# Performance work log

Hardware: AMD Instinct MI355X
Metric: run time of the kernel (lower is better)

The kernel has to match this reference:

```python
import jax, jax.numpy as jnp
import numpy as np

EPS_INTERP = 1e-8
EPS_BN = 1e-5


def _bn_relu(x, gamma, beta):
    # x: [B, C, N]; training-mode BatchNorm1d over (B, N) with biased variance
    mean = jnp.mean(x, axis=(0, 2), keepdims=True)
    var = jnp.mean((x - mean) ** 2, axis=(0, 2), keepdims=True)
    xn = (x - mean) / jnp.sqrt(var + EPS_BN)
    return jax.nn.relu(xn * gamma[None, :, None] + beta[None, :, None])


def setup_inputs() -> dict:
    key = jax.random.key(0)
    ks = jax.random.split(key, 8)
    B, N, S, D = 16, 4096, 1024, 128
    return {
        "xyz1": jax.random.normal(ks[0], (B, 3, N), jnp.float32),
        "xyz2": jax.random.normal(ks[1], (B, 3, S), jnp.float32),
        "points1": jax.random.normal(ks[2], (B, D, N), jnp.float32),
        "points2": jax.random.normal(ks[3], (B, D, S), jnp.float32),
        "w0": jax.random.normal(ks[4], (256, 512), jnp.float32) * 0.04,
        "b0": jax.random.normal(ks[5], (256,), jnp.float32) * 0.01,
        "gamma0": jnp.ones((256,), jnp.float32),
        "beta0": jnp.zeros((256,), jnp.float32),
        "w1": jax.random.normal(ks[6], (128, 256), jnp.float32) * 0.06,
        "b1": jax.random.normal(ks[7], (128,), jnp.float32) * 0.01,
        "gamma1": jnp.ones((128,), jnp.float32),
        "beta1": jnp.zeros((128,), jnp.float32),
    }


def reference(xyz1, xyz2, points1, points2, w0, b0, gamma0, beta0, w1, b1, gamma1, beta1):
    # to [B, N, C] layouts
    x1 = jnp.transpose(xyz1, (0, 2, 1))   # [B, N, 3]
    x2 = jnp.transpose(xyz2, (0, 2, 1))   # [B, S, 3]
    p2 = jnp.transpose(points2, (0, 2, 1))  # [B, S, D]
    B, N, _ = x1.shape

    # squared pairwise distances [B, N, S]
    dists = (jnp.sum(x1 ** 2, -1)[:, :, None]
             + jnp.sum(x2 ** 2, -1)[:, None, :]
             - 2.0 * jnp.einsum('bnc,bsc->bns', x1, x2))

    # 3 nearest neighbors (ascending distance)
    neg_d, idx = jax.lax.top_k(-dists, 3)   # idx: [B, N, 3]
    d3 = -neg_d
    recip = 1.0 / (d3 + EPS_INTERP)
    weight = recip / jnp.sum(recip, axis=2, keepdims=True)  # [B, N, 3]

    # gather neighbor features: [B, N, 3, D]
    gathered = jax.vmap(lambda p, i: p[i])(p2, idx)
    # NOTE: this repo flattens the 3 weighted neighbors (no sum) -> [B, N, 3*D]
    interp = (gathered * weight[..., None]).reshape(B, N, -1)

    new_pts = jnp.concatenate([jnp.transpose(points1, (0, 2, 1)), interp], axis=-1)  # [B, N, 512]
    x = jnp.transpose(new_pts, (0, 2, 1))  # [B, 512, N]

    x = _bn_relu(jnp.einsum('oc,bcn->bon', w0, x) + b0[None, :, None], gamma0, beta0)
    x = _bn_relu(jnp.einsum('oc,bcn->bon', w1, x) + b1[None, :, None], gamma1, beta1)
    return x
```

## Files before the change

### kernel.cpp

```cpp
#include <hip/hip_runtime.h>
#include <stdint.h>

typedef unsigned short ushort_t;
typedef __attribute__((ext_vector_type(8))) __bf16 bf16x8;
typedef __attribute__((ext_vector_type(4))) float f32x4;

__device__ __forceinline__ float b2f(ushort_t u) {
    unsigned v = ((unsigned)u) << 16;
    float f;
    __builtin_memcpy(&f, &v, 4);
    return f;
}

__device__ __forceinline__ ushort_t f2b(float f) {
    __bf16 h = (__bf16)f;
    return __builtin_bit_cast(ushort_t, h);
}

__device__ __forceinline__ void gl_lds16(const void* g, void* l) {
    __builtin_amdgcn_global_load_lds((const __attribute__((address_space(1))) void*)g,
                                     (__attribute__((address_space(3))) void*)l, 16, 0, 0);
}

__global__ __launch_bounds__(256) void k_pre(const float* __restrict__ w0, ushort_t* __restrict__ w0b,
                                             const float* __restrict__ w1, ushort_t* __restrict__ w1b,
                                             const float* __restrict__ xyz2, float4* __restrict__ sdat,
                                             const float* __restrict__ points2, ushort_t* __restrict__ p2t,
                                             float* __restrict__ zb) {
    int bid = blockIdx.x;
    int t = threadIdx.x;
    if (bid < 512) {
        int i = bid * 256 + t;
        w0b[i] = f2b(w0[i]);
    } else if (bid < 640) {
        int i = (bid - 512) * 256 + t;
        w1b[i] = f2b(w1[i]);
    } else if (bid < 704) {
        int bb = bid - 640;
        int b = bb & 15, by = bb >> 4;
        int s = by * 256 + t;
        const float* x2 = xyz2 + (size_t)b * 3 * 1024;
        float x = x2[s], y = x2[1024 + s], z = x2[2048 + s];
        float4 v;
        v.x = x; v.y = y; v.z = z;
        v.w = __fadd_rn(__fadd_rn(__fmul_rn(x, x), __fmul_rn(y, y)), __fmul_rn(z, z));
        sdat[(size_t)b * 1024 + s] = v;
    } else if (bid < 960) {
        int bb = bid - 704;
        int b = bb & 15, sy = bb >> 4;
        int s = sy * 64 + (t & 63);
        int g = t >> 6;
        const float* src = points2 + (size_t)b * 128 * 1024 + s;
        ushort_t* dst = p2t + ((size_t)b * 1024 + s) * 128;
#pragma unroll
        for (int i = 0; i < 4; ++i) {
            int cp = i * 4 + g;
            ushort_t tmp[8];
#pragma unroll
            for (int k = 0; k < 8; ++k) tmp[k] = f2b(src[(size_t)(cp * 8 + k) * 1024]);
            *(uint4*)(dst + cp * 8) = *(const uint4*)tmp;
        }
    } else {
        zb[t] = 0.f; zb[256 + t] = 0.f;
        if (t < 128) { zb[512 + t] = 0.f; zb[640 + t] = 0.f; }
    }
}

__global__ __launch_bounds__(256) void k_interp(const float* __restrict__ xyz1,
                                                const float4* __restrict__ sdat,
                                                const float* __restrict__ points1,
                                                const ushort_t* __restrict__ p2t,
                                                ushort_t* __restrict__ X) {
    int b = blockIdx.x;
    int n0 = blockIdx.y * 32;
    int t = threadIdx.x;
    int tq = t & 31;
    int slice = t >> 5;
    int wave = t >> 6, lane = t & 63;

    __shared__ __align__(16) char sbuf[16384];
    float4* sP = (float4*)sbuf;
    int*   sidx = (int*)sbuf;
    float* sw   = (float*)(sbuf + 384);
    __shared__ float sD[768];
    __shared__ int   sI[768];

    {
        const float4* src = sdat + (size_t)b * 1024;
#pragma unroll
        for (int c = 0; c < 4; ++c) {
            int p = wave * 256 + c * 64 + lane;
            gl_lds16(src + p, sbuf + p * 16);
        }
    }

    int n = n0 + tq;
    float x = xyz1[((size_t)b * 3 + 0) * 4096 + n];
    float y = xyz1[((size_t)b * 3 + 1) * 4096 + n];
    float z = xyz1[((size_t)b * 3 + 2) * 4096 + n];
    float s1 = __fadd_rn(__fadd_rn(__fmul_rn(x, x), __fmul_rn(y, y)), __fmul_rn(z, z));

    __syncthreads();

    const float* p1base = points1 + (size_t)b * 128 * 4096 + n0 + tq;
    float p1v[16];
#pragma unroll
    for (int i = 0; i < 2; ++i)
#pragma unroll
        for (int k = 0; k < 8; ++k)
            p1v[i * 8 + k] = p1base[(size_t)(((i * 8 + slice) * 8) + k) * 4096];

    float d0 = 1e30f, d1 = 1e30f, d2 = 1e30f;
    int i0 = 0, i1 = 0, i2 = 0;
    int sbeg = slice * 128;
    const float4* sdL = sP + sbeg;
#pragma unroll 8
    for (int s = 0; s < 128; ++s) {
        float4 v = sdL[s];
        float dot = fmaf(z, v.z, fmaf(y, v.y, __fmul_rn(x, v.x)));
        float d = __fadd_rn(fmaf(-2.0f, dot, s1), v.w);
        int si = sbeg + s;
        bool c0 = d < d0, c1 = d < d1, c2 = d < d2;
        i2 = c1 ? i1 : (c2 ? si : i2);
        i1 = c0 ? i0 : (c1 ? si : i1);
        i0 = c0 ? si : i0;
        d2 = fminf(fmaxf(d, d1), d2);
        d1 = fminf(fmaxf(d, d0), d1);
        d0 = fminf(d, d0);
    }
    sD[t * 3 + 0] = d0; sD[t * 3 + 1] = d1; sD[t * 3 + 2] = d2;
    sI[t * 3 + 0] = i0; sI[t * 3 + 1] = i1; sI[t * 3 + 2] = i2;

    {
        ushort_t* dstbase = X + (size_t)(b * 4096 + n0 + tq) * 512;
#pragma unroll
        for (int i = 0; i < 2; ++i) {
            int piece = i * 8 + slice;
            ushort_t tmp[8];
#pragma unroll
            for (int k = 0; k < 8; ++k) tmp[k] = f2b(p1v[i * 8 + k]);
            *(uint4*)(dstbase + piece * 8) = *(const uint4*)tmp;
        }
    }
    __syncthreads();

    if (t < 32) {
        int sel0 = -1, sel1 = -1;
        float seld[3]; int seli[3];
#pragma unroll
        for (int r = 0; r < 3; ++r) {
            float bd = 1e38f; int bi = 1 << 30;
            for (int k = 0; k < 24; ++k) {
                int s3 = (k * 0xAAAB) >> 17;
                int rank = k - s3 * 3;
                int base = (s3 * 32 + t) * 3 + rank;
                float cd = sD[base];
                int ci = sI[base];
                bool excl = (ci == sel0) | (ci == sel1);
                bool better = (!excl) & ((cd < bd) | ((cd == bd) & (ci < bi)));
                if (better) { bd = cd; bi = ci; }
            }
            seld[r] = bd; seli[r] = bi;
            if (r == 0) sel0 = bi; else if (r == 1) sel1 = bi;
        }
        float r0 = 1.0f / (seld[0] + 1e-8f);
        float r1 = 1.0f / (seld[1] + 1e-8f);
        float r2 = 1.0f / (seld[2] + 1e-8f);
        float rs = r0 + r1 + r2;
        sw[t * 3 + 0] = r0 / rs; sw[t * 3 + 1] = r1 / rs; sw[t * 3 + 2] = r2 / rs;
        sidx[t * 3 + 0] = seli[0]; sidx[t * 3 + 1] = seli[1]; sidx[t * 3 + 2] = seli[2];
    }
    __syncthreads();

#pragma unroll
    for (int i = 0; i < 6; ++i) {
        int idx = i * 256 + t;
        int q = idx / 48;
        int rem = idx - q * 48;
        int r = rem >> 4;
        int piece = rem & 15;
        int si = sidx[q * 3 + r] & 1023;
        float wt = sw[q * 3 + r];
        const ushort_t* src = p2t + ((size_t)b * 1024 + si) * 128 + piece * 8;
        uint4 raw = *(const uint4*)src;
        ushort_t* e = (ushort_t*)&raw;
        ushort_t outv[8];
#pragma unroll
        for (int k = 0; k < 8; ++k) outv[k] = f2b(wt * b2f(e[k]));
        ushort_t* dst = X + (size_t)(b * 4096 + n0 + q) * 512 + 128 + r * 128 + piece * 8;
        *(uint4*)dst = *(const uint4*)outv;
    }
}

__global__ __launch_bounds__(512, 4) void k_gemm(const ushort_t* __restrict__ A,
                                                 const ushort_t* __restrict__ Bt,
                                                 const float* __restrict__ bias,
                                                 ushort_t* __restrict__ Y,
                                                 float* __restrict__ gs,
                                                 float* __restrict__ gq,
                                                 int Mtot, int K) {
    __shared__ __align__(16) char smem[51200];
    ushort_t* As = (ushort_t*)smem;
    ushort_t* Bs = (ushort_t*)(smem + 32768);
    ushort_t* sY = (ushort_t*)smem;
    float* red_s = (float*)(smem + 49152);
    float* red_q = red_s + 256;

    int t = threadIdx.x;
    int j0 = blockIdx.x * 128;
    int wave = t >> 6, lane = t & 63;
    int wm = wave >> 1, wn = wave & 1;
    int l16 = lane & 15, quad = lane >> 4;
    int sw7 = l16 & 7;

    if (t < 256) { red_s[t] = 0.f; red_q[t] = 0.f; }

    f32x4 acc[4][4] = {};

    int nk = K >> 6;
    for (int kt = 0; kt < nk; ++kt) {
#pragma unroll
        for (int c = 0; c < 4; ++c) {
            int idx = c * 512 + t;
            int row = idx >> 3, kc = idx & 7;
            gl_lds16(A + (size_t)row * K + kt * 64 + ((kc ^ (row & 7)) * 8), As + idx * 8);
        }
#pragma unroll
        for (int c = 0; c < 2; ++c) {
            int idx = c * 512 + t;
            int row = idx >> 3, kc = idx & 7;
            gl_lds16(Bt + (size_t)(j0 + row) * K + kt * 64 + ((kc ^ (row & 7)) * 8), Bs + idx * 8);
        }
        __syncthreads();

#pragma unroll
        for (int kk = 0; kk < 2; ++kk) {
            bf16x8 af[4], bfr[4];
#pragma unroll
            for (int mi = 0; mi < 4; ++mi)
                af[mi] = *(const bf16x8*)(As + (wm * 64 + mi * 16 + l16) * 64 + (((kk * 4 + quad) ^ sw7) * 8));
#pragma unroll
            for (int ni = 0; ni < 4; ++ni)
                bfr[ni] = *(const bf16x8*)(Bs + (wn * 64 + ni * 16 + l16) * 64 + (((kk * 4 + quad) ^ sw7) * 8));
#pragma unroll
            for (int mi = 0; mi < 4; ++mi)
#pragma unroll
                for (int ni = 0; ni < 4; ++ni)
                    acc[mi][ni] = __builtin_amdgcn_mfma_f32_16x16x32_bf16(af[mi], bfr[ni], acc[mi][ni], 0, 0, 0);
        }
        __syncthreads();
    }

#pragma unroll
    for (int h = 0; h < 2; ++h) {
        if ((wm >> 1) == h) {
#pragma unroll
            for (int mi = 0; mi < 4; ++mi) {
                int obase = wm * 64 + mi * 16 + quad * 4;
                int ocol = obase - h * 128;
                float bv[4];
#pragma unroll
                for (int r = 0; r < 4; ++r) bv[r] = bias[obase + r];
                float sr[4] = {0.f, 0.f, 0.f, 0.f}, qr[4] = {0.f, 0.f, 0.f, 0.f};
#pragma unroll
                for (int ni = 0; ni < 4; ++ni) {
                    int j_local = wn * 64 + ni * 16 + l16;
                    ushort4 pk;
                    float v0 = acc[mi][ni][0] + bv[0];
                    float v1 = acc[mi][ni][1] + bv[1];
                    float v2 = acc[mi][ni][2] + bv[2];
                    float v3 = acc[mi][ni][3] + bv[3];
                    pk.x = f2b(v0); pk.y = f2b(v1); pk.z = f2b(v2); pk.w = f2b(v3);
                    sr[0] += v0; qr[0] += v0 * v0;
                    sr[1] += v1; qr[1] += v1 * v1;
                    sr[2] += v2; qr[2] += v2 * v2;
                    sr[3] += v3; qr[3] += v3 * v3;
                    *(ushort4*)(sY + j_local * 136 + ocol) = pk;
                }
#pragma unroll
                for (int r = 0; r < 4; ++r) {
                    float s = sr[r], q = qr[r];
                    s += __shfl_xor(s, 1); s += __shfl_xor(s, 2);
                    s += __shfl_xor(s, 4); s += __shfl_xor(s, 8);
                    q += __shfl_xor(q, 1); q += __shfl_xor(q, 2);
                    q += __shfl_xor(q, 4); q += __shfl_xor(q, 8);
                    if (l16 == 0) {
                        atomicAdd(&red_s[obase + r], s);
                        atomicAdd(&red_q[obase + r], q);
                    }
                }
            }
        }
        __syncthreads();
#pragma unroll
        for (int rep = 0; rep < 4; ++rep) {
            int idx = rep * 512 + t;
            int jl = idx >> 4;
            int o8 = idx & 15;
            uint4 vv = *(const uint4*)(sY + jl * 136 + o8 * 8);
            *(uint4*)(Y + (size_t)(j0 + jl) * Mtot + h * 128 + o8 * 8) = vv;
        }
        __syncthreads();
    }
    if (t < 256) {
        atomicAdd(&gs[t], red_s[t]);
        atomicAdd(&gq[t], red_q[t]);
    }
}

__global__ __launch_bounds__(256) void k_gemmf(const ushort_t* __restrict__ A,
                                               const ushort_t* __restrict__ Y0,
                                               const float* __restrict__ bias,
                                               const float* __restrict__ gamma0,
                                               const float* __restrict__ beta0,
                                               const float* __restrict__ gs0,
                                               const float* __restrict__ gq0,
                                               ushort_t* __restrict__ Y,
                                               float* __restrict__ gs1,
                                               float* __restrict__ gq1,
                                               int Mtot, int K) {
    __shared__ __align__(16) char smem[35840];
    ushort_t* As = (ushort_t*)smem;
    ushort_t* Bs = (ushort_t*)(smem + 16384);
    float* sa = (float*)(smem + 32768);
    float* sb = (float*)(smem + 33792);
    ushort_t* sY = (ushort_t*)smem;
    float* red_s = (float*)(smem + 34816);
    float* red_q = red_s + 128;

    int t = threadIdx.x;
    int m0 = blockIdx.x * 128;
    int j0 = blockIdx.y * 128;
    int wave = t >> 6, lane = t & 63;
    int wm = wave >> 1, wn = wave & 1;
    int l16 = lane & 15, quad = lane >> 4;
    int sw7 = l16 & 7;

    {
        float s = gs0[t], q = gq0[t];
        float mean = s * (1.0f / 65536.0f);
        float var = q * (1.0f / 65536.0f) - mean * mean;
        float sc = gamma0[t] / sqrtf(var + 1e-5f);
        sa[t] = sc;
        sb[t] = beta0[t] - mean * sc;
    }
    if (t < 128) { red_s[t] = 0.f; red_q[t] = 0.f; }
    __syncthreads();

    f32x4 acc[4][4] = {};

    int nk = K >> 6;
    for (int kt = 0; kt < nk; ++kt) {
#pragma unroll
        for (int c = 0; c < 4; ++c) {
            int idx = c * 256 + t;
            int row = idx >> 3, kc = idx & 7;
            gl_lds16(A + (size_t)(m0 + row) * K + kt * 64 + ((kc ^ (row & 7)) * 8), As + idx * 8);
        }
#pragma unroll
        for (int c = 0; c < 4; ++c) {
            int idx = c * 256 + t;
            int row = idx >> 3, kc = idx & 7;
            int cbase = kt * 64 + kc * 8;
            uint4 raw = *(const uint4*)(Y0 + (size_t)(j0 + row) * K + cbase);
            ushort_t* e = (ushort_t*)&raw;
            ushort_t outv[8];
#pragma unroll
            for (int k = 0; k < 8; ++k) {
                float v = fmaxf(sa[cbase + k] * b2f(e[k]) + sb[cbase + k], 0.f);
                outv[k] = f2b(v);
            }
            *(uint4*)(Bs + row * 64 + ((kc ^ (row & 7)) * 8)) = *(const uint4*)outv;
        }
        __syncthreads();

#pragma unroll
        for (int kk = 0; kk < 2; ++kk) {
            bf16x8 af[4], bfr[4];
#pragma unroll
            for (int mi = 0; mi < 4; ++mi)
                af[mi] = *(const bf16x8*)(As + (wm * 64 + mi * 16 + l16) * 64 + (((kk * 4 + quad) ^ sw7) * 8));
#pragma unroll
            for (int ni = 0; ni < 4; ++ni)
                bfr[ni] = *(const bf16x8*)(Bs + (wn * 64 + ni * 16 + l16) * 64 + (((kk * 4 + quad) ^ sw7) * 8));
#pragma unroll
            for (int mi = 0; mi < 4; ++mi)
#pragma unroll
                for (int ni = 0; ni < 4; ++ni)
                    acc[mi][ni] = __builtin_amdgcn_mfma_f32_16x16x32_bf16(af[mi], bfr[ni], acc[mi][ni], 0, 0, 0);
        }
        __syncthreads();
    }

#pragma unroll
    for (int mi = 0; mi < 4; ++mi) {
        int obase = wm * 64 + mi * 16 + quad * 4;
        float bv[4];
#pragma unroll
        for (int r = 0; r < 4; ++r) bv[r] = bias[m0 + obase + r];
        float sr[4] = {0.f, 0.f, 0.f, 0.f}, qr[4] = {0.f, 0.f, 0.f, 0.f};
#pragma unroll
        for (int ni = 0; ni < 4; ++ni) {
            int j_local = wn * 64 + ni * 16 + l16;
            ushort4 pk;
            float v0 = acc[mi][ni][0] + bv[0];
            float v1 = acc[mi][ni][1] + bv[1];
            float v2 = acc[mi][ni][2] + bv[2];
            float v3 = acc[mi][ni][3] + bv[3];
            pk.x = f2b(v0); pk.y = f2b(v1); pk.z = f2b(v2); pk.w = f2b(v3);
            sr[0] += v0; qr[0] += v0 * v0;
            sr[1] += v1; qr[1] += v1 * v1;
            sr[2] += v2; qr[2] += v2 * v2;
            sr[3] += v3; qr[3] += v3 * v3;
            *(ushort4*)(sY + j_local * 136 + obase) = pk;
        }
#pragma unroll
        for (int r = 0; r < 4; ++r) {
            float s = sr[r], q = qr[r];
            s += __shfl_xor(s, 1); s += __shfl_xor(s, 2);
            s += __shfl_xor(s, 4); s += __shfl_xor(s, 8);
            q += __shfl_xor(q, 1); q += __shfl_xor(q, 2);
            q += __shfl_xor(q, 4); q += __shfl_xor(q, 8);
            if (l16 == 0) {
                atomicAdd(&red_s[obase + r], s);
                atomicAdd(&red_q[obase + r], q);
            }
        }
    }
    __syncthreads();

#pragma unroll
    for (int rep = 0; rep < 8; ++rep) {
        int idx = rep * 256 + t;
        int jl = idx >> 4;
        int o8 = idx & 15;
        uint4 vv = *(const uint4*)(sY + jl * 136 + o8 * 8);
        *(uint4*)(Y + (size_t)(j0 + jl) * Mtot + m0 + o8 * 8) = vv;
    }
    if (t < 128) {
        atomicAdd(&gs1[m0 + t], red_s[t]);
        atomicAdd(&gq1[m0 + t], red_q[t]);
    }
}

__global__ __launch_bounds__(256) void k_out(const ushort_t* __restrict__ Y1,
                                             const float* __restrict__ gs1,
                                             const float* __restrict__ gq1,
                                             const float* __restrict__ gamma1,
                                             const float* __restrict__ beta1,
                                             float* __restrict__ out) {
    __shared__ float sa[128], sb[128];
    int t = threadIdx.x;
    if (t < 128) {
        float s = gs1[t], q = gq1[t];
        float mean = s * (1.0f / 65536.0f);
        float var = q * (1.0f / 65536.0f) - mean * mean;
        float sc = gamma1[t] / sqrtf(var + 1e-5f);
        sa[t] = sc;
        sb[t] = beta1[t] - mean * sc;
    }
    __syncthreads();
    int b = blockIdx.x;
    int nl = t & 127;
    int half = t >> 7;
    int n = blockIdx.y * 128 + nl;
    const uint4* src = (const uint4*)(Y1 + (size_t)(b * 4096 + n) * 128);
    float* dst = out + (size_t)b * 128 * 4096 + n;
    uint4 raw[8];
#pragma unroll
    for (int p = 0; p < 8; ++p) raw[p] = src[half * 8 + p];
    const ushort_t* e = (const ushort_t*)raw;
#pragma unroll
    for (int c = 0; c < 64; ++c) {
        int ch = half * 64 + c;
        float v = b2f(e[c]);
        v = fmaxf(sa[ch] * v + sb[ch], 0.f);
        dst[(size_t)ch * 4096] = v;
    }
}

extern "C" void kernel_launch(void* const* d_in, const int* in_sizes, int n_in,
                              void* d_out, int out_size, void* d_ws, size_t ws_size,
                              hipStream_t stream) {
    const float* xyz1    = (const float*)d_in[0];
    const float* xyz2    = (const float*)d_in[1];
    const float* points1 = (const float*)d_in[2];
    const float* points2 = (const float*)d_in[3];
    const float* w0      = (const float*)d_in[4];
    const float* b0      = (const float*)d_in[5];
    const float* gamma0  = (const float*)d_in[6];
    const float* beta0   = (const float*)d_in[7];
    const float* w1      = (const float*)d_in[8];
    const float* b1      = (const float*)d_in[9];
    const float* gamma1  = (const float*)d_in[10];
    const float* beta1   = (const float*)d_in[11];
    float* out = (float*)d_out;

    char* ws = (char*)d_ws;
    const size_t OFF_X    = 0;
    const size_t OFF_Y0   = 67108864;
    const size_t OFF_Y1   = 100663296;
    const size_t OFF_P2T  = 117440512;
    const size_t OFF_W0B  = 121634816;
    const size_t OFF_W1B  = 121896960;
    const size_t OFF_AB   = 121962496;
    const size_t OFF_SDAT = 121965568;

    ushort_t* X    = (ushort_t*)(ws + OFF_X);
    ushort_t* Y0   = (ushort_t*)(ws + OFF_Y0);
    ushort_t* Y1   = (ushort_t*)(ws + OFF_Y1);
    ushort_t* p2t  = (ushort_t*)(ws + OFF_P2T);
    ushort_t* w0b  = (ushort_t*)(ws + OFF_W0B);
    ushort_t* w1b  = (ushort_t*)(ws + OFF_W1B);
    float* ab      = (float*)(ws + OFF_AB);
    float4* sdat   = (float4*)(ws + OFF_SDAT);
    float* gs0 = ab;        float* gq0 = ab + 256;
    float* gs1 = ab + 512;  float* gq1 = ab + 640;

    k_pre<<<961, 256, 0, stream>>>(w0, w0b, w1, w1b, xyz2, sdat, points2, p2t, ab);
    k_interp<<<dim3(16, 128), 256, 0, stream>>>(xyz1, sdat, points1, p2t, X);
    k_gemm<<<512, 512, 0, stream>>>(w0b, X, b0, Y0, gs0, gq0, 256, 512);
    k_gemmf<<<dim3(1, 512), 256, 0, stream>>>(w1b, Y0, b1, gamma0, beta0, gs0, gq0, Y1, gs1, gq1, 128, 256);
    k_out<<<dim3(16, 32), 256, 0, stream>>>(Y1, gs1, gq1, gamma1, beta1, out);
}
```

Measured before the change: 218.6 us.

## Halve GEMM column tiles and spread BN stat atomics over eight copies

Both GEMM kernels now use 64-column tiles instead of 128, which doubles the grid to 1024 blocks and shrinks LDS use so more blocks fit per CU. The first GEMM writes all 256 output rows in a single epilogue pass instead of two halves. BatchNorm sum and sum-of-squares atomics are spread across 8 copies indexed by block, and consumers add the copies together, to cut contention on the global atomics. The cost is less data reuse per tile (the weight tile is reloaded twice as often) and slightly more work to reduce the statistics.

```diff
diff --git a/kernel.cpp b/kernel.cpp
--- a/kernel.cpp
+++ b/kernel.cpp
@@ -61,8 +61,7 @@
             *(uint4*)(dst + cp * 8) = *(const uint4*)tmp;
         }
     } else {
-        zb[t] = 0.f; zb[256 + t] = 0.f;
-        if (t < 128) { zb[512 + t] = 0.f; zb[640 + t] = 0.f; }
+        for (int i = t; i < 6144; i += 256) zb[i] = 0.f;
     }
 }
 
@@ -192,22 +191,22 @@
     }
 }
 
-__global__ __launch_bounds__(512, 4) void k_gemm(const ushort_t* __restrict__ A,
+__global__ __launch_bounds__(512, 6) void k_gemm(const ushort_t* __restrict__ A,
                                                  const ushort_t* __restrict__ Bt,
                                                  const float* __restrict__ bias,
                                                  ushort_t* __restrict__ Y,
                                                  float* __restrict__ gs,
                                                  float* __restrict__ gq,
                                                  int Mtot, int K) {
-    __shared__ __align__(16) char smem[51200];
+    __shared__ __align__(16) char smem[43008];
     ushort_t* As = (ushort_t*)smem;
     ushort_t* Bs = (ushort_t*)(smem + 32768);
     ushort_t* sY = (ushort_t*)smem;
-    float* red_s = (float*)(smem + 49152);
+    float* red_s = (float*)(smem + 40960);
     float* red_q = red_s + 256;
 
     int t = threadIdx.x;
-    int j0 = blockIdx.x * 128;
+    int j0 = blockIdx.x * 64;
     int wave = t >> 6, lane = t & 63;
     int wm = wave >> 1, wn = wave & 1;
     int l16 = lane & 15, quad = lane >> 4;
@@ -215,7 +214,7 @@
 
     if (t < 256) { red_s[t] = 0.f; red_q[t] = 0.f; }
 
-    f32x4 acc[4][4] = {};
+    f32x4 acc[4][2] = {};
 
     int nk = K >> 6;
     for (int kt = 0; kt < nk; ++kt) {
@@ -225,9 +224,8 @@
             int row = idx >> 3, kc = idx & 7;
             gl_lds16(A + (size_t)row * K + kt * 64 + ((kc ^ (row & 7)) * 8), As + idx * 8);
         }
-#pragma unroll
-        for (int c = 0; c < 2; ++c) {
-            int idx = c * 512 + t;
+        {
+            int idx = t;
             int row = idx >> 3, kc = idx & 7;
             gl_lds16(Bt + (size_t)(j0 + row) * K + kt * 64 + ((kc ^ (row & 7)) * 8), Bs + idx * 8);
         }
@@ -235,109 +233,105 @@
 
 #pragma unroll
         for (int kk = 0; kk < 2; ++kk) {
-            bf16x8 af[4], bfr[4];
+            bf16x8 af[4], bfr[2];
 #pragma unroll
             for (int mi = 0; mi < 4; ++mi)
                 af[mi] = *(const bf16x8*)(As + (wm * 64 + mi * 16 + l16) * 64 + (((kk * 4 + quad) ^ sw7) * 8));
 #pragma unroll
-            for (int ni = 0; ni < 4; ++ni)
-                bfr[ni] = *(const bf16x8*)(Bs + (wn * 64 + ni * 16 + l16) * 64 + (((kk * 4 + quad) ^ sw7) * 8));
+            for (int ni = 0; ni < 2; ++ni)
+                bfr[ni] = *(const bf16x8*)(Bs + (wn * 32 + ni * 16 + l16) * 64 + (((kk * 4 + quad) ^ sw7) * 8));
 #pragma unroll
             for (int mi = 0; mi < 4; ++mi)
 #pragma unroll
-                for (int ni = 0; ni < 4; ++ni)
+                for (int ni = 0; ni < 2; ++ni)
                     acc[mi][ni] = __builtin_amdgcn_mfma_f32_16x16x32_bf16(af[mi], bfr[ni], acc[mi][ni], 0, 0, 0);
         }
         __syncthreads();
     }
 
 #pragma unroll
-    for (int h = 0; h < 2; ++h) {
-        if ((wm >> 1) == h) {
-#pragma unroll
-            for (int mi = 0; mi < 4; ++mi) {
-                int obase = wm * 64 + mi * 16 + quad * 4;
-                int ocol = obase - h * 128;
-                float bv[4];
-#pragma unroll
-                for (int r = 0; r < 4; ++r) bv[r] = bias[obase + r];
-                float sr[4] = {0.f, 0.f, 0.f, 0.f}, qr[4] = {0.f, 0.f, 0.f, 0.f};
-#pragma unroll
-                for (int ni = 0; ni < 4; ++ni) {
-                    int j_local = wn * 64 + ni * 16 + l16;
-                    ushort4 pk;
-                    float v0 = acc[mi][ni][0] + bv[0];
-                    float v1 = acc[mi][ni][1] + bv[1];
-                    float v2 = acc[mi][ni][2] + bv[2];
-                    float v3 = acc[mi][ni][3] + bv[3];
-                    pk.x = f2b(v0); pk.y = f2b(v1); pk.z = f2b(v2); pk.w = f2b(v3);
-                    sr[0] += v0; qr[0] += v0 * v0;
-                    sr[1] += v1; qr[1] += v1 * v1;
-                    sr[2] += v2; qr[2] += v2 * v2;
-                    sr[3] += v3; qr[3] += v3 * v3;
-                    *(ushort4*)(sY + j_local * 136 + ocol) = pk;
-                }
-#pragma unroll
-                for (int r = 0; r < 4; ++r) {
-                    float s = sr[r], q = qr[r];
-                    s += __shfl_xor(s, 1); s += __shfl_xor(s, 2);
-                    s += __shfl_xor(s, 4); s += __shfl_xor(s, 8);
-                    q += __shfl_xor(q, 1); q += __shfl_xor(q, 2);
-                    q += __shfl_xor(q, 4); q += __shfl_xor(q, 8);
-                    if (l16 == 0) {
-                        atomicAdd(&red_s[obase + r], s);
-                        atomicAdd(&red_q[obase + r], q);
-                    }
-                }
+    for (int mi = 0; mi < 4; ++mi) {
+        int obase = wm * 64 + mi * 16 + quad * 4;
+        float bv[4];
+#pragma unroll
+        for (int r = 0; r < 4; ++r) bv[r] = bias[obase + r];
+        float sr[4] = {0.f, 0.f, 0.f, 0.f}, qr[4] = {0.f, 0.f, 0.f, 0.f};
+#pragma unroll
+        for (int ni = 0; ni < 2; ++ni) {
+            int j_local = wn * 32 + ni * 16 + l16;
+            ushort4 pk;
+            float v0 = acc[mi][ni][0] + bv[0];
+            float v1 = acc[mi][ni][1] + bv[1];
+            float v2 = acc[mi][ni][2] + bv[2];
+            float v3 = acc[mi][ni][3] + bv[3];
+            pk.x = f2b(v0); pk.y = f2b(v1); pk.z = f2b(v2); pk.w = f2b(v3);
+            sr[0] += v0; qr[0] += v0 * v0;
+            sr[1] += v1; qr[1] += v1 * v1;
+            sr[2] += v2; qr[2] += v2 * v2;
+            sr[3] += v3; qr[3] += v3 * v3;
+            *(ushort4*)(sY + j_local * 264 + obase) = pk;
+        }
+#pragma unroll
+        for (int r = 0; r < 4; ++r) {
+            float s = sr[r], q = qr[r];
+            s += __shfl_xor(s, 1); s += __shfl_xor(s, 2);
+            s += __shfl_xor(s, 4); s += __shfl_xor(s, 8);
+            q += __shfl_xor(q, 1); q += __shfl_xor(q, 2);
+            q += __shfl_xor(q, 4); q += __shfl_xor(q, 8);
+            if (l16 == 0) {
+                atomicAdd(&red_s[obase + r], s);
+                atomicAdd(&red_q[obase + r], q);
             }
         }
-        __syncthreads();
-#pragma unroll
-        for (int rep = 0; rep < 4; ++rep) {
-            int idx = rep * 512 + t;
-            int jl = idx >> 4;
-            int o8 = idx & 15;
-            uint4 vv = *(const uint4*)(sY + jl * 136 + o8 * 8);
-            *(uint4*)(Y + (size_t)(j0 + jl) * Mtot + h * 128 + o8 * 8) = vv;
-        }
-        __syncthreads();
+    }
+    __syncthreads();
+
+#pragma unroll
+    for (int rep = 0; rep < 4; ++rep) {
+        int idx = rep * 512 + t;
+        int jl = idx >> 5;
+        int o8 = idx & 31;
+        uint4 vv = *(const uint4*)(sY + jl * 264 + o8 * 8);
+        *(uint4*)(Y + (size_t)(j0 + jl) * Mtot + o8 * 8) = vv;
     }
     if (t < 256) {
-        atomicAdd(&gs[t], red_s[t]);
-        atomicAdd(&gq[t], red_q[t]);
-    }
-}
-
-__global__ __launch_bounds__(256) void k_gemmf(const ushort_t* __restrict__ A,
-                                               const ushort_t* __restrict__ Y0,
-                                               const float* __restrict__ bias,
-                                               const float* __restrict__ gamma0,
-                                               const float* __restrict__ beta0,
-                                               const float* __restrict__ gs0,
-                                               const float* __restrict__ gq0,
-                                               ushort_t* __restrict__ Y,
-                                               float* __restrict__ gs1,
-                                               float* __restrict__ gq1,
-                                               int Mtot, int K) {
-    __shared__ __align__(16) char smem[35840];
+        int cp = blockIdx.x & 7;
+        atomicAdd(&gs[cp * 256 + t], red_s[t]);
+        atomicAdd(&gq[cp * 256 + t], red_q[t]);
+    }
+}
+
+__global__ __launch_bounds__(256, 4) void k_gemmf(const ushort_t* __restrict__ A,
+                                                  const ushort_t* __restrict__ Y0,
+                                                  const float* __restrict__ bias,
+                                                  const float* __restrict__ gamma0,
+                                                  const float* __restrict__ beta0,
+                                                  const float* __restrict__ gs0,
+                                                  const float* __restrict__ gq0,
+                                                  ushort_t* __restrict__ Y,
+                                                  float* __restrict__ gs1,
+                                                  float* __restrict__ gq1,
+                                                  int Mtot, int K) {
+    __shared__ __align__(16) char smem[27648];
     ushort_t* As = (ushort_t*)smem;
     ushort_t* Bs = (ushort_t*)(smem + 16384);
-    float* sa = (float*)(smem + 32768);
-    float* sb = (float*)(smem + 33792);
     ushort_t* sY = (ushort_t*)smem;
-    float* red_s = (float*)(smem + 34816);
+    float* sa = (float*)(smem + 24576);
+    float* sb = (float*)(smem + 25600);
+    float* red_s = (float*)(smem + 26624);
     float* red_q = red_s + 128;
 
     int t = threadIdx.x;
-    int m0 = blockIdx.x * 128;
-    int j0 = blockIdx.y * 128;
+    int j0 = blockIdx.x * 64;
     int wave = t >> 6, lane = t & 63;
     int wm = wave >> 1, wn = wave & 1;
     int l16 = lane & 15, quad = lane >> 4;
     int sw7 = l16 & 7;
 
     {
-        float s = gs0[t], q = gq0[t];
+        float s = 0.f, q = 0.f;
+#pragma unroll
+        for (int k = 0; k < 8; ++k) { s += gs0[k * 256 + t]; q += gq0[k * 256 + t]; }
         float mean = s * (1.0f / 65536.0f);
         float var = q * (1.0f / 65536.0f) - mean * mean;
         float sc = gamma0[t] / sqrtf(var + 1e-5f);
@@ -347,7 +341,7 @@
     if (t < 128) { red_s[t] = 0.f; red_q[t] = 0.f; }
     __syncthreads();
 
-    f32x4 acc[4][4] = {};
+    f32x4 acc[4][2] = {};
 
     int nk = K >> 6;
     for (int kt = 0; kt < nk; ++kt) {
@@ -355,10 +349,10 @@
         for (int c = 0; c < 4; ++c) {
             int idx = c * 256 + t;
             int row = idx >> 3, kc = idx & 7;
-            gl_lds16(A + (size_t)(m0 + row) * K + kt * 64 + ((kc ^ (row & 7)) * 8), As + idx * 8);
-        }
-#pragma unroll
-        for (int c = 0; c < 4; ++c) {
+            gl_lds16(A + (size_t)row * K + kt * 64 + ((kc ^ (row & 7)) * 8), As + idx * 8);
+        }
+#pragma unroll
+        for (int c = 0; c < 2; ++c) {
             int idx = c * 256 + t;
             int row = idx >> 3, kc = idx & 7;
             int cbase = kt * 64 + kc * 8;
@@ -376,17 +370,17 @@
 
 #pragma unroll
         for (int kk = 0; kk < 2; ++kk) {
-            bf16x8 af[4], bfr[4];
+            bf16x8 af[4], bfr[2];
 #pragma unroll
             for (int mi = 0; mi < 4; ++mi)
                 af[mi] = *(const bf16x8*)(As + (wm * 64 + mi * 16 + l16) * 64 + (((kk * 4 + quad) ^ sw7) * 8));
 #pragma unroll
-            for (int ni = 0; ni < 4; ++ni)
-                bfr[ni] = *(const bf16x8*)(Bs + (wn * 64 + ni * 16 + l16) * 64 + (((kk * 4 + quad) ^ sw7) * 8));
+            for (int ni = 0; ni < 2; ++ni)
+                bfr[ni] = *(const bf16x8*)(Bs + (wn * 32 + ni * 16 + l16) * 64 + (((kk * 4 + quad) ^ sw7) * 8));
 #pragma unroll
             for (int mi = 0; mi < 4; ++mi)
 #pragma unroll
-                for (int ni = 0; ni < 4; ++ni)
+                for (int ni = 0; ni < 2; ++ni)
                     acc[mi][ni] = __builtin_amdgcn_mfma_f32_16x16x32_bf16(af[mi], bfr[ni], acc[mi][ni], 0, 0, 0);
         }
         __syncthreads();
@@ -397,11 +391,11 @@
         int obase = wm * 64 + mi * 16 + quad * 4;
         float bv[4];
 #pragma unroll
-        for (int r = 0; r < 4; ++r) bv[r] = bias[m0 + obase + r];
+        for (int r = 0; r < 4; ++r) bv[r] = bias[obase + r];
         float sr[4] = {0.f, 0.f, 0.f, 0.f}, qr[4] = {0.f, 0.f, 0.f, 0.f};
 #pragma unroll
-        for (int ni = 0; ni < 4; ++ni) {
-            int j_local = wn * 64 + ni * 16 + l16;
+        for (int ni = 0; ni < 2; ++ni) {
+            int j_local = wn * 32 + ni * 16 + l16;
             ushort4 pk;
             float v0 = acc[mi][ni][0] + bv[0];
             float v1 = acc[mi][ni][1] + bv[1];
@@ -430,16 +424,17 @@
     __syncthreads();
 
 #pragma unroll
-    for (int rep = 0; rep < 8; ++rep) {
+    for (int rep = 0; rep < 4; ++rep) {
         int idx = rep * 256 + t;
         int jl = idx >> 4;
         int o8 = idx & 15;
         uint4 vv = *(const uint4*)(sY + jl * 136 + o8 * 8);
-        *(uint4*)(Y + (size_t)(j0 + jl) * Mtot + m0 + o8 * 8) = vv;
+        *(uint4*)(Y + (size_t)(j0 + jl) * Mtot + o8 * 8) = vv;
     }
     if (t < 128) {
-        atomicAdd(&gs1[m0 + t], red_s[t]);
-        atomicAdd(&gq1[m0 + t], red_q[t]);
+        int cp = blockIdx.x & 7;
+        atomicAdd(&gs1[cp * 128 + t], red_s[t]);
+        atomicAdd(&gq1[cp * 128 + t], red_q[t]);
     }
 }
 
@@ -452,7 +447,9 @@
     __shared__ float sa[128], sb[128];
     int t = threadIdx.x;
     if (t < 128) {
-        float s = gs1[t], q = gq1[t];
+        float s = 0.f, q = 0.f;
+#pragma unroll
+        for (int k = 0; k < 8; ++k) { s += gs1[k * 128 + t]; q += gq1[k * 128 + t]; }
         float mean = s * (1.0f / 65536.0f);
         float var = q * (1.0f / 65536.0f) - mean * mean;
         float sc = gamma1[t] / sqrtf(var + 1e-5f);
@@ -503,8 +500,8 @@
     const size_t OFF_P2T  = 117440512;
     const size_t OFF_W0B  = 121634816;
     const size_t OFF_W1B  = 121896960;
-    const size_t OFF_AB   = 121962496;
     const size_t OFF_SDAT = 121965568;
+    const size_t OFF_AB   = 122227712;
 
     ushort_t* X    = (ushort_t*)(ws + OFF_X);
     ushort_t* Y0   = (ushort_t*)(ws + OFF_Y0);
@@ -512,14 +509,14 @@
     ushort_t* p2t  = (ushort_t*)(ws + OFF_P2T);
     ushort_t* w0b  = (ushort_t*)(ws + OFF_W0B);
     ushort_t* w1b  = (ushort_t*)(ws + OFF_W1B);
+    float4* sdat   = (float4*)(ws + OFF_SDAT);
     float* ab      = (float*)(ws + OFF_AB);
-    float4* sdat   = (float4*)(ws + OFF_SDAT);
-    float* gs0 = ab;        float* gq0 = ab + 256;
-    float* gs1 = ab + 512;  float* gq1 = ab + 640;
+    float* gs0 = ab;               float* gq0 = ab + 2048;
+    float* gs1 = ab + 4096;        float* gq1 = ab + 5120;
 
     k_pre<<<961, 256, 0, stream>>>(w0, w0b, w1, w1b, xyz2, sdat, points2, p2t, ab);
     k_interp<<<dim3(16, 128), 256, 0, stream>>>(xyz1, sdat, points1, p2t, X);
-    k_gemm<<<512, 512, 0, stream>>>(w0b, X, b0, Y0, gs0, gq0, 256, 512);
-    k_gemmf<<<dim3(1, 512), 256, 0, stream>>>(w1b, Y0, b1, gamma0, beta0, gs0, gq0, Y1, gs1, gq1, 128, 256);
+    k_gemm<<<1024, 512, 0, stream>>>(w0b, X, b0, Y0, gs0, gq0, 256, 512);
+    k_gemmf<<<1024, 256, 0, stream>>>(w1b, Y0, b1, gamma0, beta0, gs0, gq0, Y1, gs1, gq1, 128, 256);
     k_out<<<dim3(16, 32), 256, 0, stream>>>(Y1, gs1, gq1, gamma1, beta1, out);
 }
```

Result: no change. 217.2 us (-0.7%).

## Spread BN stat atomics over 8 copies and drop LDS XOR swizzle

Applied to the files above, without the earlier changes.

The global BatchNorm sum and sum-of-squares accumulators are split into 8 copies indexed by block, and the consumers add the copies together. This is meant to reduce atomic contention on a single address per channel. Separately, the XOR swizzle on the LDS tiles in both GEMMs is removed in favour of plain row-major indexing, which simplifies address math but may bring back LDS bank conflicts on the 128-byte-stride fragment reads. The workspace layout is adjusted to hold the larger accumulator buffer, which k_pre now zeroes in a loop.

```diff
diff --git a/kernel.cpp b/kernel.cpp
--- a/kernel.cpp
+++ b/kernel.cpp
@@ -61,8 +61,7 @@
             *(uint4*)(dst + cp * 8) = *(const uint4*)tmp;
         }
     } else {
-        zb[t] = 0.f; zb[256 + t] = 0.f;
-        if (t < 128) { zb[512 + t] = 0.f; zb[640 + t] = 0.f; }
+        for (int i = t; i < 6144; i += 256) zb[i] = 0.f;
     }
 }
 
@@ -211,7 +210,6 @@
     int wave = t >> 6, lane = t & 63;
     int wm = wave >> 1, wn = wave & 1;
     int l16 = lane & 15, quad = lane >> 4;
-    int sw7 = l16 & 7;
 
     if (t < 256) { red_s[t] = 0.f; red_q[t] = 0.f; }
 
@@ -223,13 +221,13 @@
         for (int c = 0; c < 4; ++c) {
             int idx = c * 512 + t;
             int row = idx >> 3, kc = idx & 7;
-            gl_lds16(A + (size_t)row * K + kt * 64 + ((kc ^ (row & 7)) * 8), As + idx * 8);
+            gl_lds16(A + (size_t)row * K + kt * 64 + kc * 8, As + idx * 8);
         }
 #pragma unroll
         for (int c = 0; c < 2; ++c) {
             int idx = c * 512 + t;
             int row = idx >> 3, kc = idx & 7;
-            gl_lds16(Bt + (size_t)(j0 + row) * K + kt * 64 + ((kc ^ (row & 7)) * 8), Bs + idx * 8);
+            gl_lds16(Bt + (size_t)(j0 + row) * K + kt * 64 + kc * 8, Bs + idx * 8);
         }
         __syncthreads();
 
@@ -238,10 +236,10 @@
             bf16x8 af[4], bfr[4];
 #pragma unroll
             for (int mi = 0; mi < 4; ++mi)
-                af[mi] = *(const bf16x8*)(As + (wm * 64 + mi * 16 + l16) * 64 + (((kk * 4 + quad) ^ sw7) * 8));
+                af[mi] = *(const bf16x8*)(As + (wm * 64 + mi * 16 + l16) * 64 + kk * 32 + quad * 8);
 #pragma unroll
             for (int ni = 0; ni < 4; ++ni)
-                bfr[ni] = *(const bf16x8*)(Bs + (wn * 64 + ni * 16 + l16) * 64 + (((kk * 4 + quad) ^ sw7) * 8));
+                bfr[ni] = *(const bf16x8*)(Bs + (wn * 64 + ni * 16 + l16) * 64 + kk * 32 + quad * 8);
 #pragma unroll
             for (int mi = 0; mi < 4; ++mi)
 #pragma unroll
@@ -303,8 +301,9 @@
         __syncthreads();
     }
     if (t < 256) {
-        atomicAdd(&gs[t], red_s[t]);
-        atomicAdd(&gq[t], red_q[t]);
+        int cp = blockIdx.x & 7;
+        atomicAdd(&gs[cp * 256 + t], red_s[t]);
+        atomicAdd(&gq[cp * 256 + t], red_q[t]);
     }
 }
 
@@ -334,10 +333,11 @@
     int wave = t >> 6, lane = t & 63;
     int wm = wave >> 1, wn = wave & 1;
     int l16 = lane & 15, quad = lane >> 4;
-    int sw7 = l16 & 7;
 
     {
-        float s = gs0[t], q = gq0[t];
+        float s = 0.f, q = 0.f;
+#pragma unroll
+        for (int k = 0; k < 8; ++k) { s += gs0[k * 256 + t]; q += gq0[k * 256 + t]; }
         float mean = s * (1.0f / 65536.0f);
         float var = q * (1.0f / 65536.0f) - mean * mean;
         float sc = gamma0[t] / sqrtf(var + 1e-5f);
@@ -355,7 +355,7 @@
         for (int c = 0; c < 4; ++c) {
             int idx = c * 256 + t;
             int row = idx >> 3, kc = idx & 7;
-            gl_lds16(A + (size_t)(m0 + row) * K + kt * 64 + ((kc ^ (row & 7)) * 8), As + idx * 8);
+            gl_lds16(A + (size_t)(m0 + row) * K + kt * 64 + kc * 8, As + idx * 8);
         }
 #pragma unroll
         for (int c = 0; c < 4; ++c) {
@@ -370,7 +370,7 @@
                 float v = fmaxf(sa[cbase + k] * b2f(e[k]) + sb[cbase + k], 0.f);
                 outv[k] = f2b(v);
             }
-            *(uint4*)(Bs + row * 64 + ((kc ^ (row & 7)) * 8)) = *(const uint4*)outv;
+            *(uint4*)(Bs + idx * 8) = *(const uint4*)outv;
         }
         __syncthreads();
 
@@ -379,10 +379,10 @@
             bf16x8 af[4], bfr[4];
 #pragma unroll
             for (int mi = 0; mi < 4; ++mi)
-                af[mi] = *(const bf16x8*)(As + (wm * 64 + mi * 16 + l16) * 64 + (((kk * 4 + quad) ^ sw7) * 8));
+                af[mi] = *(const bf16x8*)(As + (wm * 64 + mi * 16 + l16) * 64 + kk * 32 + quad * 8);
 #pragma unroll
             for (int ni = 0; ni < 4; ++ni)
-                bfr[ni] = *(const bf16x8*)(Bs + (wn * 64 + ni * 16 + l16) * 64 + (((kk * 4 + quad) ^ sw7) * 8));
+                bfr[ni] = *(const bf16x8*)(Bs + (wn * 64 + ni * 16 + l16) * 64 + kk * 32 + quad * 8);
 #pragma unroll
             for (int mi = 0; mi < 4; ++mi)
 #pragma unroll
@@ -438,8 +438,9 @@
         *(uint4*)(Y + (size_t)(j0 + jl) * Mtot + m0 + o8 * 8) = vv;
     }
     if (t < 128) {
-        atomicAdd(&gs1[m0 + t], red_s[t]);
-        atomicAdd(&gq1[m0 + t], red_q[t]);
+        int cp = blockIdx.y & 7;
+        atomicAdd(&gs1[cp * 128 + m0 + t], red_s[t]);
+        atomicAdd(&gq1[cp * 128 + m0 + t], red_q[t]);
     }
 }
 
@@ -452,7 +453,9 @@
     __shared__ float sa[128], sb[128];
     int t = threadIdx.x;
     if (t < 128) {
-        float s = gs1[t], q = gq1[t];
+        float s = 0.f, q = 0.f;
+#pragma unroll
+        for (int k = 0; k < 8; ++k) { s += gs1[k * 128 + t]; q += gq1[k * 128 + t]; }
         float mean = s * (1.0f / 65536.0f);
         float var = q * (1.0f / 65536.0f) - mean * mean;
         float sc = gamma1[t] / sqrtf(var + 1e-5f);
@@ -503,8 +506,8 @@
     const size_t OFF_P2T  = 117440512;
     const size_t OFF_W0B  = 121634816;
     const size_t OFF_W1B  = 121896960;
-    const size_t OFF_AB   = 121962496;
     const size_t OFF_SDAT = 121965568;
+    const size_t OFF_AB   = 122227712;
 
     ushort_t* X    = (ushort_t*)(ws + OFF_X);
     ushort_t* Y0   = (ushort_t*)(ws + OFF_Y0);
@@ -512,10 +515,10 @@
     ushort_t* p2t  = (ushort_t*)(ws + OFF_P2T);
     ushort_t* w0b  = (ushort_t*)(ws + OFF_W0B);
     ushort_t* w1b  = (ushort_t*)(ws + OFF_W1B);
+    float4* sdat   = (float4*)(ws + OFF_SDAT);
     float* ab      = (float*)(ws + OFF_AB);
-    float4* sdat   = (float4*)(ws + OFF_SDAT);
-    float* gs0 = ab;        float* gq0 = ab + 256;
-    float* gs1 = ab + 512;  float* gq1 = ab + 640;
+    float* gs0 = ab;               float* gq0 = ab + 2048;
+    float* gs1 = ab + 4096;        float* gq1 = ab + 5120;
 
     k_pre<<<961, 256, 0, stream>>>(w0, w0b, w1, w1b, xyz2, sdat, points2, p2t, ab);
     k_interp<<<dim3(16, 128), 256, 0, stream>>>(xyz1, sdat, points1, p2t, X);
```

Measured after the change: 204.2 us. 6.6% less time.
